# Kernel tuning notes

Hardware: AMD Instinct MI355X
Metric: run time of the kernel (lower is better)

Reference implementation:

```python
import jax, jax.numpy as jnp
import numpy as np

SIGNAL_SIZE = 33554432  # 2**25
N_ELEMENTS = 25         # log2(SIGNAL_SIZE)


def fft_shift(a, shift):
    # Faithful port of the torch fft_shift (note: 'shift' variable is reused
    # in the original; the phase ramp overwrites it after shift_samples).
    shift = 1.0 - shift
    n_samples = a.shape[-1]
    shift_samples = shift * n_samples * 0.5
    spec = jnp.fft.rfft(a, norm='ortho')
    n_coeffs = spec.shape[-1]
    phase = jnp.arange(n_coeffs) * (2j * np.pi / n_coeffs)  # complex64 ramp
    spec = spec * jnp.exp(phase * shift_samples)
    return jnp.fft.irfft(spec, n=n_samples, norm='ortho')


def setup_inputs() -> dict:
    key = jax.random.key(0)
    elements = jax.random.uniform(key, (N_ELEMENTS,), minval=-1.0, maxval=1.0,
                                  dtype=jnp.float32)
    return {"elements": elements}


def reference(elements):
    # dirac impulse of size 2 at position 0
    signal = jnp.zeros(2, dtype=jnp.float32).at[0].set(1.0)
    for i in range(N_ELEMENTS):  # fixed trip count; sizes double each step
        if i > 0:
            new_signal = jnp.zeros(signal.shape[-1] * 2, dtype=signal.dtype)
            signal = new_signal.at[::2].set(signal)
        shift_factor = 1.0 / (2 ** i)
        signal = fft_shift(signal, elements[i] * shift_factor)
    return signal  # shape [SIGNAL_SIZE]
```

## Files before the change

kernel.cpp:

```cpp
#include <hip/hip_runtime.h>


constexpr float PI_F    = 3.14159265358979323846f;
constexpr float TWOPI_F = 6.28318530717958647692f;
constexpr unsigned M24 = 1u << 24;

__device__ __forceinline__ void phase_sincos(float th, float* sn, float* cs) {
    double d = (double)th * 0.15915494309189533577;
    d -= rint(d);
    float ang = (float)(d * 6.2831853071795864769);
    __sincosf(ang, sn, cs);
}

__global__ __launch_bounds__(256) void build_q(const float* __restrict__ el,
                                               float2* __restrict__ Q) {
    __shared__ float c_s[18], s_s[18], T_s[18];
    int tid = threadIdx.x;
    if (tid < 18) {
        float e = el[tid];
        float shift1 = e * (1.0f / (float)(1u << tid));
        float sh2 = 1.0f - shift1;
        float s = sh2 * (float)(1u << tid);
        float c = (float)(6.2831853071795864769 / (double)((1u << tid) + 1u));
        c_s[tid] = c;
        s_s[tid] = s;
        float p  = (float)(1u << tid) * c;
        float th = p * s;
        float sn, cs; phase_sincos(th, &sn, &cs);
        T_s[tid] = cs;
    }
    __syncthreads();

    unsigned r = blockIdx.x * 256u + (unsigned)tid;
    if (r == 0u) { Q[0] = make_float2(1.0f, 0.0f); return; }

    unsigned t = (unsigned)__builtin_ctz(r);
    float Pr = T_s[t], Pi = 0.0f;

#pragma unroll
    for (int i = 1; i <= 17; ++i) {
        unsigned hi = 1u << i;
        int sd = (int)((r + hi) & (2u * hi - 1u)) - (int)hi;
        int K  = (i <= (int)t) ? 0 : (sd < 0 ? -sd : sd);
        float sgn = (sd < 0) ? -1.0f : 1.0f;
        float p  = (float)K * c_s[i];
        float th = p * s_s[i];
        float sn, cs; phase_sincos(th, &sn, &cs);
        float ssn = sgn * sn;
        float nr = Pr * cs - Pi * ssn;
        float ni = Pr * ssn + Pi * cs;
        Pr = nr; Pi = ni;
    }
    Q[r] = make_float2(Pr, Pi);
}

struct WPair { float2 wk, wmk; };

__device__ __forceinline__ WPair chain_W(unsigned k,
                                         const float* __restrict__ c_s,
                                         const float* __restrict__ s_s,
                                         const float* __restrict__ T_s,
                                         const float2* __restrict__ Q) {
    const float sc = 1.0f / 33554432.0f;
    unsigned t = (unsigned)__builtin_ctz(k);
    unsigned r = k & 0x3FFFFu;
    float Pr, Pi;
    if (r != 0u) {
        float2 q = Q[r];
        Pr = q.x; Pi = q.y;
    } else {
        Pr = T_s[t]; Pi = 0.0f;
    }

#pragma unroll
    for (int i = 18; i <= 23; ++i) {
        unsigned hi = 1u << i;
        int sd = (int)((k + hi) & (2u * hi - 1u)) - (int)hi;
        int K  = (i <= (int)t) ? 0 : (sd < 0 ? -sd : sd);
        float sgn = (sd < 0) ? -1.0f : 1.0f;
        float p  = (float)K * c_s[i];
        float th = p * s_s[i];
        float sn, cs; phase_sincos(th, &sn, &cs);
        float ssn = sgn * sn;
        float nr = Pr * cs - Pi * ssn;
        float ni = Pr * ssn + Pi * cs;
        Pr = nr; Pi = ni;
    }

    unsigned mk = M24 - k;
    float thk = ((float)k  * c_s[24]) * s_s[24];
    float thm = ((float)mk * c_s[24]) * s_s[24];
    float snk, csk, snm, csm;
    phase_sincos(thk, &snk, &csk);
    phase_sincos(thm, &snm, &csm);

    float Skr = Pr * csk - Pi * snk;
    float Ski = Pr * snk + Pi * csk;
    float Smr = Pr * csm + Pi * snm;
    float Smi = Pr * snm - Pi * csm;

    float Ar = Skr + Smr, Ai = Ski - Smi;
    float Br = Skr - Smr, Bi = Ski + Smi;
    float ang = (float)k * (TWOPI_F / 33554432.0f);
    float ts, tc; __sincosf(ang, &ts, &tc);
    float Cr = tc * Br - ts * Bi;
    float Ci = ts * Br + tc * Bi;

    WPair w;
    w.wk  = make_float2((Ar - Ci) * sc, (Ai + Cr) * sc);
    w.wmk = make_float2((Ar + Ci) * sc, (Cr - Ai) * sc);
    return w;
}

__device__ __forceinline__ void bf4(float2* __restrict__ row, int e0, int d,
                                    float2 tw, float2 tw2) {
    float2 x0 = row[e0], x1 = row[e0 + d], x2 = row[e0 + 2*d], x3 = row[e0 + 3*d];
    float2 a0 = make_float2(x0.x + x2.x, x0.y + x2.y);
    float2 d0 = make_float2(x0.x - x2.x, x0.y - x2.y);
    float2 a1 = make_float2(x1.x + x3.x, x1.y + x3.y);
    float2 d1 = make_float2(x1.x - x3.x, x1.y - x3.y);
    float2 a2 = make_float2(d0.x * tw.x - d0.y * tw.y,  d0.x * tw.y + d0.y * tw.x);
    float2 a3 = make_float2(-d1.x * tw.y - d1.y * tw.x, d1.x * tw.x - d1.y * tw.y);
    row[e0]       = make_float2(a0.x + a1.x, a0.y + a1.y);
    float2 u1 = make_float2(a0.x - a1.x, a0.y - a1.y);
    row[e0 + d]   = make_float2(u1.x * tw2.x - u1.y * tw2.y, u1.x * tw2.y + u1.y * tw2.x);
    row[e0 + 2*d] = make_float2(a2.x + a3.x, a2.y + a3.y);
    float2 u3 = make_float2(a2.x - a3.x, a2.y - a3.y);
    row[e0 + 3*d] = make_float2(u3.x * tw2.x - u3.y * tw2.y, u3.x * tw2.y + u3.y * tw2.x);
}

__device__ __forceinline__ void fft256x16_inv(float2 (*lds)[257], int tid) {
    {
        int j2 = tid & 63;
        float s, c; __sincosf((PI_F / 128.0f) * (float)j2, &s, &c);
        float2 tw  = make_float2(c, s);
        float2 tw2 = make_float2(c * c - s * s, 2.0f * c * s);
        __syncthreads();
#pragma unroll
        for (int v = 0; v < 4; ++v) {
            int row = (tid >> 6) + 4 * v;
            bf4(lds[row], j2, 64, tw, tw2);
        }
    }
    {
        int rowb = tid & 15;
        int j2   = tid >> 4;
        float s, c; __sincosf((PI_F / 32.0f) * (float)j2, &s, &c);
        float2 tw  = make_float2(c, s);
        float2 tw2 = make_float2(c * c - s * s, 2.0f * c * s);
        __syncthreads();
#pragma unroll
        for (int v = 0; v < 4; ++v) {
            bf4(lds[rowb], 64 * v + j2, 16, tw, tw2);
        }
    }
    {
        int rowb = tid & 15;
        int j2   = tid >> 6;
        int bbl  = (tid >> 4) & 3;
        float s, c; __sincosf((PI_F / 8.0f) * (float)j2, &s, &c);
        float2 tw  = make_float2(c, s);
        float2 tw2 = make_float2(c * c - s * s, 2.0f * c * s);
        __syncthreads();
#pragma unroll
        for (int v = 0; v < 4; ++v) {
            int bb = bbl + 4 * v;
            bf4(lds[rowb], 16 * bb + j2, 4, tw, tw2);
        }
    }
    {
        int rowb = tid & 15;
        int bbl  = tid >> 4;
        __syncthreads();
#pragma unroll
        for (int v = 0; v < 4; ++v) {
            int e0 = 4 * (bbl + 16 * v);
            float2* row = lds[rowb];
            float2 x0 = row[e0], x1 = row[e0 + 1], x2 = row[e0 + 2], x3 = row[e0 + 3];
            float2 a0 = make_float2(x0.x + x2.x, x0.y + x2.y);
            float2 d0 = make_float2(x0.x - x2.x, x0.y - x2.y);
            float2 a1 = make_float2(x1.x + x3.x, x1.y + x3.y);
            float2 d1 = make_float2(x1.x - x3.x, x1.y - x3.y);
            row[e0]     = make_float2(a0.x + a1.x, a0.y + a1.y);
            row[e0 + 1] = make_float2(a0.x - a1.x, a0.y - a1.y);
            row[e0 + 2] = make_float2(d0.x - d1.y, d0.y + d1.x);
            row[e0 + 3] = make_float2(d0.x + d1.y, d0.y - d1.x);
        }
    }
    __syncthreads();
}

__device__ __forceinline__ int c_of_row(int b, int r) {
    if (b == 0) {
        if (r < 8)  return r;
        if (r == 8) return 32768;
        return 65536 - (r - 8);
    }
    return (r < 8) ? (8 * b + r) : (65536 - 8 * b - (r - 8));
}

__global__ __launch_bounds__(256, 4) void fused_build_fft_a(const float* __restrict__ el,
                                                            const float2* __restrict__ Q,
                                                            float2* __restrict__ out) {
    __shared__ float2 lds[16][257];
    __shared__ float c_s[25], s_s[25], T_s[24];
    int tid = threadIdx.x;
    if (tid < 25) {
        float e = el[tid];
        float shift1 = e * (1.0f / (float)(1u << tid));
        float sh2 = 1.0f - shift1;
        float s = sh2 * (float)(1u << tid);
        float c = (float)(6.2831853071795864769 / (double)((1u << tid) + 1u));
        c_s[tid] = c;
        s_s[tid] = s;
        if (tid < 24) {
            float p  = (float)(1u << tid) * c;
            float th = p * s;
            float sn, cs; phase_sincos(th, &sn, &cs);
            T_s[tid] = cs;
        }
    }
    __syncthreads();

    int b   = blockIdx.x;
    int r   = tid & 15;
    int k30 = tid >> 4;
    int c   = c_of_row(b, r);
    int rm  = (b == 0 && (r == 0 || r == 8)) ? r : (r ^ 8);

#pragma unroll 1
    for (int u = 0; u < 8; ++u) {
        int k3 = k30 + 16 * u;
        unsigned j = (unsigned)c + ((unsigned)k3 << 16);
        if (b == 0 && r == 0 && k3 == 0) {
            float p  = 16777216.0f * c_s[24];
            float th = p * s_s[24];
            float sn, cs; phase_sincos(th, &sn, &cs);
            const float sc = 1.0f / 33554432.0f;
            lds[0][0] = make_float2((1.0f + cs) * sc, (1.0f - cs) * sc);
            WPair w = chain_W(8388608u, c_s, s_s, T_s, Q);
            lds[0][128] = w.wk;
        } else {
            WPair w = chain_W(j, c_s, s_s, T_s, Q);
            lds[r][k3] = w.wk;
            int k3m = (b == 0 && r == 0) ? (256 - k3) : (255 - k3);
            lds[rm][k3m] = w.wmk;
        }
    }

    fft256x16_inv(lds, tid);

#pragma unroll
    for (int u = 0; u < 16; ++u) {
        int e = tid + 256 * u;
        int row = e & 15, p = e >> 4;
        int t3 = (int)(__brev((unsigned)p) >> 24);
        int cr = c_of_row(b, row);
        out[cr + (t3 << 16)] = lds[row][p];
    }
}

__global__ __launch_bounds__(256) void fft_stage_b(const float2* __restrict__ in,
                                                   float2* __restrict__ out) {
    __shared__ float2 lds[16][257];
    int tid = threadIdx.x;
    int wg  = blockIdx.x;
    int k1b = (wg & 15) * 16;
    int t3  = wg >> 4;
    const float tsc = TWOPI_F / 65536.0f;
    {
        int row = tid & 15;
        int k20 = tid >> 4;
        float sb, cb; __sincosf(tsc * (float)(t3 * k20), &sb, &cb);
        float ss, cs; __sincosf(tsc * (float)(t3 * 16), &ss, &cs);
        float2 w = make_float2(cb, sb);
#pragma unroll
        for (int u = 0; u < 16; ++u) {
            int k2 = k20 + 16 * u;
            float2 v = in[k1b + row + (k2 << 8) + (t3 << 16)];
            lds[row][k2] = make_float2(v.x * w.x - v.y * w.y, v.x * w.y + v.y * w.x);
            float nx = w.x * cs - w.y * ss;
            float ny = w.x * ss + w.y * cs;
            w = make_float2(nx, ny);
        }
    }
    fft256x16_inv(lds, tid);
#pragma unroll
    for (int u = 0; u < 16; ++u) {
        int e = tid + 256 * u;
        int row = e & 15, p = e >> 4;
        int t2 = (int)(__brev((unsigned)p) >> 24);
        out[k1b + row + (t2 << 8) + (t3 << 16)] = lds[row][p];
    }
}

__global__ __launch_bounds__(256) void fft_stage_c(const float2* __restrict__ in,
                                                   float2* __restrict__ out) {
    __shared__ float2 lds[16][257];
    int tid = threadIdx.x;
    int wg  = blockIdx.x;
    int t3b = (wg & 15) * 16;
    int t2  = wg >> 4;
    const float tsc = TWOPI_F / 16777216.0f;
    {
        int k1 = tid;
        int base = (t3b + (t2 << 8)) * k1;
        float sb, cb; __sincosf(tsc * (float)base, &sb, &cb);
        float ss, cs; __sincosf(tsc * (float)k1, &ss, &cs);
        float2 w = make_float2(cb, sb);
#pragma unroll
        for (int u = 0; u < 16; ++u) {
            float2 v = in[k1 + (t2 << 8) + ((t3b + u) << 16)];
            lds[u][k1] = make_float2(v.x * w.x - v.y * w.y, v.x * w.y + v.y * w.x);
            float nx = w.x * cs - w.y * ss;
            float ny = w.x * ss + w.y * cs;
            w = make_float2(nx, ny);
        }
    }
    fft256x16_inv(lds, tid);
#pragma unroll
    for (int u = 0; u < 16; ++u) {
        int e = tid + 256 * u;
        int r = e & 15, p = e >> 4;
        int t1 = (int)(__brev((unsigned)p) >> 24);
        out[(t3b + r) + (t2 << 8) + (t1 << 16)] = lds[r][p];
    }
}

extern "C" void kernel_launch(void* const* d_in, const int* in_sizes, int n_in,
                              void* d_out, int out_size, void* d_ws, size_t ws_size,
                              hipStream_t stream) {
    const float* el = (const float*)d_in[0];
    float2* Gd = (float2*)d_out;
    float2* Q  = (float2*)d_ws;

    hipLaunchKernelGGL(build_q,          dim3(1024), dim3(256), 0, stream, el, Q);
    hipLaunchKernelGGL(fused_build_fft_a, dim3(4096), dim3(256), 0, stream, el, Q, Gd);
    hipLaunchKernelGGL(fft_stage_b,      dim3(4096), dim3(256), 0, stream, Gd, (float2*)d_ws);
    hipLaunchKernelGGL(fft_stage_c,      dim3(4096), dim3(256), 0, stream, (float2*)d_ws, Gd);
}
```

Measured before the change: 288.5 us.

## Share chain prefix products, swizzle blocks across XCDs, batch stage loads

In the fused build kernel, the per-element phase chain for stages 18-21 is computed once per thread and reused across its eight outputs. Only stages 22-23 and the tail are evaluated per output, which cuts sincos work. All three FFT kernels remap block indices with an XCD swizzle to improve L2 locality. Stages b and c preload all 16 global values into registers before the twiddle pass and add occupancy hints to launch bounds. The risks are higher register pressure, and the swizzle only maps correctly because the block count is a multiple of 8.

```diff
diff --git a/kernel.cpp b/kernel.cpp
--- a/kernel.cpp
+++ b/kernel.cpp
@@ -10,6 +10,15 @@
     d -= rint(d);
     float ang = (float)(d * 6.2831853071795864769);
     __sincosf(ang, sn, cs);
+}
+
+__device__ __forceinline__ float2 cmul(float2 a, float2 f) {
+    return make_float2(a.x * f.x - a.y * f.y, a.x * f.y + a.y * f.x);
+}
+
+__device__ __forceinline__ int xcd_swizzle(int b, int nblocks) {
+    int chunk = nblocks >> 3;
+    return (b & 7) * chunk + (b >> 3);
 }
 
 __global__ __launch_bounds__(256) void build_q(const float* __restrict__ el,
@@ -54,14 +63,55 @@
     Q[r] = make_float2(Pr, Pi);
 }
 
+__device__ __forceinline__ float2 chain_factor(int i, unsigned k,
+                                               const float* __restrict__ c_s,
+                                               const float* __restrict__ s_s) {
+    unsigned hi = 1u << i;
+    int sd = (int)((k + hi) & (2u * hi - 1u)) - (int)hi;
+    int K  = (sd < 0) ? -sd : sd;
+    float sgn = (sd < 0) ? -1.0f : 1.0f;
+    float p  = (float)K * c_s[i];
+    float th = p * s_s[i];
+    float sn, cs; phase_sincos(th, &sn, &cs);
+    return make_float2(cs, sgn * sn);
+}
+
 struct WPair { float2 wk, wmk; };
+
+__device__ __forceinline__ WPair chain_tail(unsigned k, float Pr, float Pi,
+                                            const float* __restrict__ c_s,
+                                            const float* __restrict__ s_s) {
+    const float sc = 1.0f / 33554432.0f;
+    unsigned mk = M24 - k;
+    float thk = ((float)k  * c_s[24]) * s_s[24];
+    float thm = ((float)mk * c_s[24]) * s_s[24];
+    float snk, csk, snm, csm;
+    phase_sincos(thk, &snk, &csk);
+    phase_sincos(thm, &snm, &csm);
+
+    float Skr = Pr * csk - Pi * snk;
+    float Ski = Pr * snk + Pi * csk;
+    float Smr = Pr * csm + Pi * snm;
+    float Smi = Pr * snm - Pi * csm;
+
+    float Ar = Skr + Smr, Ai = Ski - Smi;
+    float Br = Skr - Smr, Bi = Ski + Smi;
+    float ang = (float)k * (TWOPI_F / 33554432.0f);
+    float ts, tc; __sincosf(ang, &ts, &tc);
+    float Cr = tc * Br - ts * Bi;
+    float Ci = ts * Br + tc * Bi;
+
+    WPair w;
+    w.wk  = make_float2((Ar - Ci) * sc, (Ai + Cr) * sc);
+    w.wmk = make_float2((Ar + Ci) * sc, (Cr - Ai) * sc);
+    return w;
+}
 
 __device__ __forceinline__ WPair chain_W(unsigned k,
                                          const float* __restrict__ c_s,
                                          const float* __restrict__ s_s,
                                          const float* __restrict__ T_s,
                                          const float2* __restrict__ Q) {
-    const float sc = 1.0f / 33554432.0f;
     unsigned t = (unsigned)__builtin_ctz(k);
     unsigned r = k & 0x3FFFFu;
     float Pr, Pi;
@@ -71,7 +121,6 @@
     } else {
         Pr = T_s[t]; Pi = 0.0f;
     }
-
 #pragma unroll
     for (int i = 18; i <= 23; ++i) {
         unsigned hi = 1u << i;
@@ -86,30 +135,7 @@
         float ni = Pr * ssn + Pi * cs;
         Pr = nr; Pi = ni;
     }
-
-    unsigned mk = M24 - k;
-    float thk = ((float)k  * c_s[24]) * s_s[24];
-    float thm = ((float)mk * c_s[24]) * s_s[24];
-    float snk, csk, snm, csm;
-    phase_sincos(thk, &snk, &csk);
-    phase_sincos(thm, &snm, &csm);
-
-    float Skr = Pr * csk - Pi * snk;
-    float Ski = Pr * snk + Pi * csk;
-    float Smr = Pr * csm + Pi * snm;
-    float Smi = Pr * snm - Pi * csm;
-
-    float Ar = Skr + Smr, Ai = Ski - Smi;
-    float Br = Skr - Smr, Bi = Ski + Smi;
-    float ang = (float)k * (TWOPI_F / 33554432.0f);
-    float ts, tc; __sincosf(ang, &ts, &tc);
-    float Cr = tc * Br - ts * Bi;
-    float Ci = ts * Br + tc * Bi;
-
-    WPair w;
-    w.wk  = make_float2((Ar - Ci) * sc, (Ai + Cr) * sc);
-    w.wmk = make_float2((Ar + Ci) * sc, (Cr - Ai) * sc);
-    return w;
+    return chain_tail(k, Pr, Pi, c_s, s_s);
 }
 
 __device__ __forceinline__ void bf4(float2* __restrict__ row, int e0, int d,
@@ -222,29 +248,54 @@
     }
     __syncthreads();
 
-    int b   = blockIdx.x;
+    int b   = xcd_swizzle(blockIdx.x, 4096);
     int r   = tid & 15;
     int k30 = tid >> 4;
     int c   = c_of_row(b, r);
     int rm  = (b == 0 && (r == 0 || r == 8)) ? r : (r ^ 8);
 
+    if (b == 0 && r == 0) {
 #pragma unroll 1
-    for (int u = 0; u < 8; ++u) {
-        int k3 = k30 + 16 * u;
-        unsigned j = (unsigned)c + ((unsigned)k3 << 16);
-        if (b == 0 && r == 0 && k3 == 0) {
-            float p  = 16777216.0f * c_s[24];
-            float th = p * s_s[24];
-            float sn, cs; phase_sincos(th, &sn, &cs);
-            const float sc = 1.0f / 33554432.0f;
-            lds[0][0] = make_float2((1.0f + cs) * sc, (1.0f - cs) * sc);
-            WPair w = chain_W(8388608u, c_s, s_s, T_s, Q);
-            lds[0][128] = w.wk;
-        } else {
-            WPair w = chain_W(j, c_s, s_s, T_s, Q);
+        for (int u = 0; u < 8; ++u) {
+            int k3 = k30 + 16 * u;
+            if (k3 == 0) {
+                float p  = 16777216.0f * c_s[24];
+                float th = p * s_s[24];
+                float sn, cs; phase_sincos(th, &sn, &cs);
+                const float sc = 1.0f / 33554432.0f;
+                lds[0][0] = make_float2((1.0f + cs) * sc, (1.0f - cs) * sc);
+                WPair w = chain_W(8388608u, c_s, s_s, T_s, Q);
+                lds[0][128] = w.wk;
+            } else {
+                unsigned j = (unsigned)k3 << 16;
+                WPair w = chain_W(j, c_s, s_s, T_s, Q);
+                lds[0][k3] = w.wk;
+                lds[0][256 - k3] = w.wmk;
+            }
+        }
+    } else {
+        unsigned kbase = (unsigned)c + ((unsigned)k30 << 16);
+        unsigned rres  = kbase & 0x3FFFFu;
+        float2 P1 = Q[rres];
+        P1 = cmul(P1, chain_factor(18, kbase, c_s, s_s));
+        P1 = cmul(P1, chain_factor(19, kbase, c_s, s_s));
+        float2 P2[2], P3[4];
+#pragma unroll
+        for (int j = 0; j < 2; ++j)
+            P2[j] = cmul(P1, chain_factor(20, kbase + ((unsigned)j << 20), c_s, s_s));
+#pragma unroll
+        for (int j = 0; j < 4; ++j)
+            P3[j] = cmul(P2[j & 1], chain_factor(21, kbase + ((unsigned)j << 20), c_s, s_s));
+
+#pragma unroll 1
+        for (int u = 0; u < 8; ++u) {
+            int k3 = k30 + 16 * u;
+            unsigned k = kbase + ((unsigned)u << 20);
+            float2 P = cmul(P3[u & 3], chain_factor(22, k, c_s, s_s));
+            P = cmul(P, chain_factor(23, k, c_s, s_s));
+            WPair w = chain_tail(k, P.x, P.y, c_s, s_s);
             lds[r][k3] = w.wk;
-            int k3m = (b == 0 && r == 0) ? (256 - k3) : (255 - k3);
-            lds[rm][k3m] = w.wmk;
+            lds[rm][255 - k3] = w.wmk;
         }
     }
 
@@ -260,24 +311,28 @@
     }
 }
 
-__global__ __launch_bounds__(256) void fft_stage_b(const float2* __restrict__ in,
-                                                   float2* __restrict__ out) {
+__global__ __launch_bounds__(256, 4) void fft_stage_b(const float2* __restrict__ in,
+                                                      float2* __restrict__ out) {
     __shared__ float2 lds[16][257];
     int tid = threadIdx.x;
-    int wg  = blockIdx.x;
+    int wg  = xcd_swizzle(blockIdx.x, 4096);
     int k1b = (wg & 15) * 16;
     int t3  = wg >> 4;
     const float tsc = TWOPI_F / 65536.0f;
     {
         int row = tid & 15;
         int k20 = tid >> 4;
+        const float2* src = in + (k1b + row + (k20 << 8) + (t3 << 16));
+        float2 vbuf[16];
+#pragma unroll
+        for (int u = 0; u < 16; ++u) vbuf[u] = src[u << 12];
         float sb, cb; __sincosf(tsc * (float)(t3 * k20), &sb, &cb);
         float ss, cs; __sincosf(tsc * (float)(t3 * 16), &ss, &cs);
         float2 w = make_float2(cb, sb);
 #pragma unroll
         for (int u = 0; u < 16; ++u) {
             int k2 = k20 + 16 * u;
-            float2 v = in[k1b + row + (k2 << 8) + (t3 << 16)];
+            float2 v = vbuf[u];
             lds[row][k2] = make_float2(v.x * w.x - v.y * w.y, v.x * w.y + v.y * w.x);
             float nx = w.x * cs - w.y * ss;
             float ny = w.x * ss + w.y * cs;
@@ -294,23 +349,27 @@
     }
 }
 
-__global__ __launch_bounds__(256) void fft_stage_c(const float2* __restrict__ in,
-                                                   float2* __restrict__ out) {
+__global__ __launch_bounds__(256, 4) void fft_stage_c(const float2* __restrict__ in,
+                                                      float2* __restrict__ out) {
     __shared__ float2 lds[16][257];
     int tid = threadIdx.x;
-    int wg  = blockIdx.x;
+    int wg  = xcd_swizzle(blockIdx.x, 4096);
     int t3b = (wg & 15) * 16;
     int t2  = wg >> 4;
     const float tsc = TWOPI_F / 16777216.0f;
     {
         int k1 = tid;
+        const float2* src = in + (k1 + (t2 << 8) + (t3b << 16));
+        float2 vbuf[16];
+#pragma unroll
+        for (int u = 0; u < 16; ++u) vbuf[u] = src[u << 16];
         int base = (t3b + (t2 << 8)) * k1;
         float sb, cb; __sincosf(tsc * (float)base, &sb, &cb);
         float ss, cs; __sincosf(tsc * (float)k1, &ss, &cs);
         float2 w = make_float2(cb, sb);
 #pragma unroll
         for (int u = 0; u < 16; ++u) {
-            float2 v = in[k1 + (t2 << 8) + ((t3b + u) << 16)];
+            float2 v = vbuf[u];
             lds[u][k1] = make_float2(v.x * w.x - v.y * w.y, v.x * w.y + v.y * w.x);
             float nx = w.x * cs - w.y * ss;
             float ny = w.x * ss + w.y * cs;
@@ -334,8 +393,8 @@
     float2* Gd = (float2*)d_out;
     float2* Q  = (float2*)d_ws;
 
-    hipLaunchKernelGGL(build_q,          dim3(1024), dim3(256), 0, stream, el, Q);
+    hipLaunchKernelGGL(build_q,           dim3(1024), dim3(256), 0, stream, el, Q);
     hipLaunchKernelGGL(fused_build_fft_a, dim3(4096), dim3(256), 0, stream, el, Q, Gd);
-    hipLaunchKernelGGL(fft_stage_b,      dim3(4096), dim3(256), 0, stream, Gd, (float2*)d_ws);
-    hipLaunchKernelGGL(fft_stage_c,      dim3(4096), dim3(256), 0, stream, (float2*)d_ws, Gd);
-}
+    hipLaunchKernelGGL(fft_stage_b,       dim3(4096), dim3(256), 0, stream, Gd, (float2*)d_ws);
+    hipLaunchKernelGGL(fft_stage_c,       dim3(4096), dim3(256), 0, stream, (float2*)d_ws, Gd);
+}
```

Measured after the change: 278.4 us. 3.5% less time.
